# Kernel tuning notes

Hardware: AMD Instinct MI355X
Metric: run time of the kernel (lower is better)

The kernel has to match this reference:

```python
import jax, jax.numpy as jnp
import numpy as np

D_MODEL = 1024
NUM_HEADS = 16
HEAD_DIM = D_MODEL // NUM_HEADS  # 64
B, S = 2, 2048


def setup_inputs() -> dict:
    key = jax.random.key(0)
    k1, k2, k3, k4, k5 = jax.random.split(key, 5)
    scale = 1.0 / np.sqrt(D_MODEL)
    return {
        "x": jax.random.normal(k1, (B, S, D_MODEL), dtype=jnp.float32),
        "Wq": jax.random.normal(k2, (D_MODEL, D_MODEL), dtype=jnp.float32) * scale,
        "bq": jax.random.normal(k3, (D_MODEL,), dtype=jnp.float32) * 0.02,
        "Wv": jax.random.normal(k4, (D_MODEL, D_MODEL), dtype=jnp.float32) * scale,
        "bv": jax.random.normal(k5, (D_MODEL,), dtype=jnp.float32) * 0.02,
    }


def reference(x, Wq, bq, Wv, bv):
    b, s, _ = x.shape
    d, n = HEAD_DIM, NUM_HEADS
    # nn.Linear: y = x @ W.T + b
    Q = x @ Wq.T + bq
    # NOTE (faithful to source bug): K uses the VALUE projection, key weights unused.
    KV = x @ Wv.T + bv
    # einops 'B S (d n) -> B S d n' -> 'B n S d'  (head index n is fast-varying)
    Qh = Q.reshape(b, s, d, n).transpose(0, 3, 1, 2)   # [B, n, S, d]
    Kt = KV.reshape(b, s, d, n).transpose(0, 3, 2, 1)  # [B, n, d, S]
    Vh = KV.reshape(b, s, d, n).transpose(0, 3, 1, 2)  # [B, n, S, d]
    scores = jnp.matmul(Qh, Kt) / jnp.sqrt(jnp.float32(d))  # [B, n, S, S]
    attn = jnp.matmul(jax.nn.softmax(scores, axis=-1), Vh)  # [B, n, S, d]
    # 'B n S d -> B S (n d)'
    out = attn.transpose(0, 2, 1, 3).reshape(b, s, n * d)
    return out
```

## Files before the change

kernel.cpp:

```cpp
#include <hip/hip_runtime.h>
#include <hip/hip_bf16.h>
#include <math.h>


typedef __bf16 bf16x8 __attribute__((ext_vector_type(8)));
typedef float  f32x4  __attribute__((ext_vector_type(4)));
typedef short  s16x4  __attribute__((ext_vector_type(4)));
typedef unsigned short ushort_t;
typedef unsigned short us8 __attribute__((ext_vector_type(8)));

#define QSCALE 0.1803368801111204f

__device__ __forceinline__ unsigned short f2bf(float f) {
  unsigned int u = __builtin_bit_cast(unsigned int, f);
  u += 0x7fffu + ((u >> 16) & 1u);
  return (unsigned short)(u >> 16);
}

__device__ __forceinline__ unsigned int pk2(float a, float b) {
  unsigned int ua = __builtin_bit_cast(unsigned int, a) + 0x8000u;
  unsigned int ub = __builtin_bit_cast(unsigned int, b) + 0x8000u;
  return (ua >> 16) | (ub & 0xffff0000u);
}

__device__ __forceinline__ void gl_lds16(const void* g, void* l) {
  __builtin_amdgcn_global_load_lds(
      (const __attribute__((address_space(1))) unsigned int*)g,
      (__attribute__((address_space(3))) unsigned int*)l, 16, 0, 0);
}

__device__ __forceinline__ f32x4 mfma_k32(bf16x8 a, bf16x8 b, f32x4 c) {
  return __builtin_amdgcn_mfma_f32_16x16x32_bf16(a, b, c, 0, 0, 0);
}
__device__ __forceinline__ f32x4 mfma_k16(s16x4 a, s16x4 b, f32x4 c) {
  return __builtin_amdgcn_mfma_f32_16x16x16bf16_1k(a, b, c, 0, 0, 0);
}

__global__ __launch_bounds__(256) void cvt3_kernel(const float4* __restrict__ x,
                                                   const float4* __restrict__ wq,
                                                   const float4* __restrict__ wv,
                                                   ushort4* __restrict__ dst) {
  const int i = blockIdx.x * 256 + threadIdx.x;
  const float4 v = (i < 1048576) ? x[i]
                 : (i < 1310720) ? wq[i - 1048576]
                                 : wv[i - 1310720];
  ushort4 o;
  o.x = f2bf(v.x); o.y = f2bf(v.y); o.z = f2bf(v.z); o.w = f2bf(v.w);
  dst[i] = o;
}

__global__ __launch_bounds__(256) void proj_kernel(
    const ushort_t* __restrict__ X,
    const ushort_t* __restrict__ Wqm,
    const ushort_t* __restrict__ Wvm,
    const float*    __restrict__ bq,
    const float*    __restrict__ bv,
    ushort_t* __restrict__ Qh,
    ushort_t* __restrict__ KVh,
    ushort_t* __restrict__ KVt)
{
  __shared__ __align__(16) unsigned char lds[32768];
  const int tid = threadIdx.x;
  const int w  = tid >> 6;
  const int l  = tid & 63;
  const int lq = l >> 4;
  const int ll = l & 15;
  const bool isQ = (blockIdx.z == 0);
  const ushort_t* Wmat = isQ ? Wqm : Wvm;
  const float*    bias = isQ ? bq  : bv;
  const int m0 = blockIdx.x * 128;
  const int by = blockIdx.y;
  const int wm = (w & 1) * 64;
  const int wn = (w >> 1) * 64;

  f32x4 acc[4][4] = {};

  for (int k0 = 0; k0 < 1024; k0 += 64) {
    __syncthreads();
#pragma unroll
    for (int t = 0; t < 4; ++t) {
      const int seg = w * 4 + t;
      const int r = seg * 8 + (l >> 3);
      const int cd = (l & 7) ^ (r & 7);
      const int cg = by * 128 + r;
      const int wrow = ((cg & 63) << 4) | (cg >> 6);
      gl_lds16(X    + (size_t)(m0 + r) * 1024 + k0 + cd * 8, lds + seg * 1024);
      gl_lds16(Wmat + (size_t)wrow * 1024 + k0 + cd * 8, lds + 16384 + seg * 1024);
    }
    __syncthreads();
#pragma unroll
    for (int kb = 0; kb < 2; ++kb) {
      const int kc = kb * 4 + lq;
      bf16x8 af[4], bfr[4];
#pragma unroll
      for (int mi = 0; mi < 4; ++mi) {
        const int m = wm + mi * 16 + ll;
        af[mi] = *(const bf16x8*)(lds + m * 128 + ((kc ^ (m & 7)) * 16));
      }
#pragma unroll
      for (int ni = 0; ni < 4; ++ni) {
        const int n = wn + ni * 16 + ll;
        bfr[ni] = *(const bf16x8*)(lds + 16384 + n * 128 + ((kc ^ (n & 7)) * 16));
      }
#pragma unroll
      for (int mi = 0; mi < 4; ++mi)
#pragma unroll
        for (int ni = 0; ni < 4; ++ni)
          acc[mi][ni] = mfma_k32(af[mi], bfr[ni], acc[mi][ni]);
    }
  }

  const int hl = wn >> 6;
  const int hh = by * 2 + hl;
  const int b  = m0 >> 11;
  const int sbase = m0 & 2047;

  if (isQ) {
#pragma unroll
    for (int ni = 0; ni < 4; ++ni) {
      const int ii = ni * 16 + ll;
      const float bb = bias[(ii << 4) | hh];
#pragma unroll
      for (int mi = 0; mi < 4; ++mi)
#pragma unroll
        for (int r = 0; r < 4; ++r) {
          const int s = sbase + wm + mi * 16 + lq * 4 + r;
          const float v = acc[mi][ni][r] + bb;
          Qh[(((size_t)(b * 16 + hh)) * 2048 + s) * 64 + ii] = f2bf(v * QSCALE);
        }
    }
  } else {
    __syncthreads();
#pragma unroll
    for (int ni = 0; ni < 4; ++ni) {
      const int ii = ni * 16 + ll;
      const float bb = bias[(ii << 4) | hh];
#pragma unroll
      for (int mi = 0; mi < 4; ++mi) {
        const float v0 = acc[mi][ni][0] + bb;
        const float v1 = acc[mi][ni][1] + bb;
        const float v2 = acc[mi][ni][2] + bb;
        const float v3 = acc[mi][ni][3] + bb;
        const unsigned int u01 = pk2(v0, v1);
        const unsigned int u23 = pk2(v2, v3);
        const int sl = wm + mi * 16 + lq * 4;
        const size_t kb0 = (((size_t)(b * 16 + hh)) * 2048 + sbase + sl) * 64 + ii;
        KVh[kb0]       = (ushort_t)(u01 & 0xffffu);
        KVh[kb0 + 64]  = (ushort_t)(u01 >> 16);
        KVh[kb0 + 128] = (ushort_t)(u23 & 0xffffu);
        KVh[kb0 + 192] = (ushort_t)(u23 >> 16);
        const int g = (wm >> 2) + mi * 4 + lq;
        const int pc = (g >> 1) ^ ll;
        *(uint2*)(lds + hl * 16384 + ii * 256 + pc * 16 + (g & 1) * 8) =
            make_uint2(u01, u23);
      }
    }
    __syncthreads();
    const int row = tid >> 1;
    const int hl2 = row >> 6, ii2 = row & 63;
    const int cbase = (tid & 1) * 8;
    ushort_t* dst = KVt + (((size_t)(b * 16 + by * 2 + hl2)) * 64 + ii2) * 2048 + sbase;
#pragma unroll
    for (int cc = 0; cc < 8; ++cc) {
      const int c = cbase + cc;
      const int pc = c ^ (ii2 & 15);
      const us8 v = *(const us8*)(lds + hl2 * 16384 + ii2 * 256 + pc * 16);
      *(us8*)(dst + c * 8) = v;
    }
  }
}

__global__ __launch_bounds__(128, 2) void attn_kernel(
    const ushort_t* __restrict__ Qh,
    const ushort_t* __restrict__ KVh,
    const ushort_t* __restrict__ KVt,
    float* __restrict__ out)
{
  __shared__ __align__(16) unsigned char sm[32768];
  const int tid = threadIdx.x;
  const int w  = tid >> 6;
  const int l  = tid & 63;
  const int quad = l >> 4;
  const int ll = l & 15;
  const int bid = blockIdx.x;
  const int bh = ((bid & 7) << 2) | (bid >> 8);
  const int qt = (bid >> 3) & 31;
  const int b = bh >> 4, h = bh & 15;
  const int qw = qt * 64 + w * 32;
  const ushort_t* Qhead  = Qh  + (size_t)bh * (2048 * 64);
  const ushort_t* Khead  = KVh + (size_t)bh * (2048 * 64);
  const ushort_t* Vthead = KVt + (size_t)bh * (64 * 2048);

  bf16x8 qf[2][2];
#pragma unroll
  for (int c = 0; c < 2; ++c)
#pragma unroll
    for (int kb = 0; kb < 2; ++kb)
      qf[c][kb] = *(const bf16x8*)(Qhead + (size_t)(qw + c * 16 + ll) * 64 +
                                   kb * 32 + quad * 8);

  f32x4 O[2][4] = {};
  float l_run[2] = {0.f, 0.f};

  for (int kt = 0; kt < 16; ++kt) {
    const int sk0 = kt * 128;
    __syncthreads();
#pragma unroll
    for (int t = 0; t < 8; ++t) {
      const int seg = w * 8 + t;
      const int r = seg * 8 + (l >> 3);
      const int cd = (l & 7) ^ (r & 7);
      gl_lds16(Khead + (size_t)(sk0 + r) * 64 + cd * 8, sm + seg * 1024);
    }
#pragma unroll
    for (int t = 0; t < 8; ++t) {
      const int seg = w * 8 + t;
      const int d = seg * 4 + (l >> 4);
      const int c8 = (l & 15) ^ (d & 15);
      gl_lds16(Vthead + (size_t)d * 2048 + sk0 + c8 * 8, sm + 16384 + seg * 1024);
    }
    __syncthreads();

    f32x4 Sa[2][8] = {};
#pragma unroll
    for (int kb = 0; kb < 2; ++kb) {
      const int kc = kb * 4 + quad;
#pragma unroll
      for (int ni = 0; ni < 8; ++ni) {
        const int n = ni * 16 + ll;
        const bf16x8 ak = *(const bf16x8*)(sm + n * 128 + ((kc ^ (n & 7)) * 16));
        Sa[0][ni] = mfma_k32(ak, qf[0][kb], Sa[0][ni]);
        Sa[1][ni] = mfma_k32(ak, qf[1][kb], Sa[1][ni]);
      }
    }

    s16x4 pk[2][8];
#pragma unroll
    for (int c = 0; c < 2; ++c) {
      float ps = 0.f;
#pragma unroll
      for (int ni = 0; ni < 8; ++ni) {
        const float p0 = __builtin_amdgcn_exp2f(Sa[c][ni][0]);
        const float p1 = __builtin_amdgcn_exp2f(Sa[c][ni][1]);
        const float p2 = __builtin_amdgcn_exp2f(Sa[c][ni][2]);
        const float p3 = __builtin_amdgcn_exp2f(Sa[c][ni][3]);
        ps += (p0 + p1) + (p2 + p3);
        const uint2 uu = make_uint2(pk2(p0, p1), pk2(p2, p3));
        pk[c][ni] = __builtin_bit_cast(s16x4, uu);
      }
      ps += __shfl_xor(ps, 16);
      ps += __shfl_xor(ps, 32);
      l_run[c] += ps;
    }

#pragma unroll
    for (int ni = 0; ni < 8; ++ni) {
      const int cb = 2 * ni + (quad >> 1);
#pragma unroll
      for (int no = 0; no < 4; ++no) {
        const int row = no * 16 + ll;
        const s16x4 bv = *(const s16x4*)(sm + 16384 + row * 256 +
                                         ((cb ^ ll) * 16) + (quad & 1) * 8);
        O[0][no] = mfma_k16(pk[0][ni], bv, O[0][no]);
        O[1][no] = mfma_k16(pk[1][ni], bv, O[1][no]);
      }
    }
  }

#pragma unroll
  for (int c = 0; c < 2; ++c) {
    const float inv = 1.f / l_run[c];
    float invr[4];
#pragma unroll
    for (int r = 0; r < 4; ++r)
      invr[r] = __shfl(inv, (l & 48) + ((l & 48) >> 2) + r);
    float* op = out + ((size_t)(b * 2048) + qw + c * 16) * 1024 + h * 64;
#pragma unroll
    for (int no = 0; no < 4; ++no)
#pragma unroll
      for (int r = 0; r < 4; ++r) {
        const int q = quad * 4 + r;
        op[(size_t)q * 1024 + no * 16 + ll] = O[c][no][r] * invr[r];
      }
  }
}

extern "C" void kernel_launch(void* const* d_in, const int* in_sizes, int n_in,
                              void* d_out, int out_size, void* d_ws, size_t ws_size,
                              hipStream_t stream) {
  const float* x  = (const float*)d_in[0];
  const float* Wq = (const float*)d_in[1];
  const float* bq = (const float*)d_in[2];
  const float* Wv = (const float*)d_in[3];
  const float* bv = (const float*)d_in[4];
  float* out = (float*)d_out;
  char* ws = (char*)d_ws;

  ushort_t* xbf  = (ushort_t*)(ws);
  ushort_t* wqbf = (ushort_t*)(ws + 8388608);
  ushort_t* wvbf = (ushort_t*)(ws + 10485760);
  ushort_t* Qh   = (ushort_t*)(ws + 12582912);
  ushort_t* KVh  = (ushort_t*)(ws + 20971520);
  ushort_t* KVt  = (ushort_t*)(ws + 29360128);

  cvt3_kernel<<<6144, 256, 0, stream>>>((const float4*)x, (const float4*)Wq,
                                        (const float4*)Wv, (ushort4*)xbf);
  proj_kernel<<<dim3(32, 8, 2), 256, 0, stream>>>(xbf, wqbf, wvbf, bq, bv,
                                                  Qh, KVh, KVt);
  attn_kernel<<<1024, 128, 0, stream>>>(Qh, KVh, KVt, out);
}
```

Measured before the change: 154.8 us.

## Prefetch next K tile during softmax and split barriers with explicit waitcnts

Loads the next K tile into LDS while softmax and PV run on the current tile, and replaces __syncthreads with s_barrier plus targeted vmcnt/lgkmcnt waits so V and K loads overlap compute. It also swaps the manual bf16 packing for the hardware v_cvt_pk_bf16_f32 instruction and moves the row-sum cross-lane shuffles out of the loop to the epilogue. This adds barriers per iteration and relies on hand-counted vmcnt values that must match the issued loads. The hardware conversion rounds to nearest-even, which differs slightly from the previous add-and-truncate rounding.

```diff
diff --git a/kernel.cpp b/kernel.cpp
--- a/kernel.cpp
+++ b/kernel.cpp
@@ -21,6 +21,12 @@
   unsigned int ua = __builtin_bit_cast(unsigned int, a) + 0x8000u;
   unsigned int ub = __builtin_bit_cast(unsigned int, b) + 0x8000u;
   return (ua >> 16) | (ub & 0xffff0000u);
+}
+
+__device__ __forceinline__ unsigned int cvtpk(float lo, float hi) {
+  unsigned int r;
+  asm("v_cvt_pk_bf16_f32 %0, %1, %2" : "=v"(r) : "v"(lo), "v"(hi));
+  return r;
 }
 
 __device__ __forceinline__ void gl_lds16(const void* g, void* l) {
@@ -202,16 +208,20 @@
   f32x4 O[2][4] = {};
   float l_run[2] = {0.f, 0.f};
 
+#pragma unroll
+  for (int t = 0; t < 8; ++t) {
+    const int seg = w * 8 + t;
+    const int r = seg * 8 + (l >> 3);
+    const int cd = (l & 7) ^ (r & 7);
+    gl_lds16(Khead + (size_t)r * 64 + cd * 8, sm + seg * 1024);
+  }
+
   for (int kt = 0; kt < 16; ++kt) {
     const int sk0 = kt * 128;
-    __syncthreads();
-#pragma unroll
-    for (int t = 0; t < 8; ++t) {
-      const int seg = w * 8 + t;
-      const int r = seg * 8 + (l >> 3);
-      const int cd = (l & 7) ^ (r & 7);
-      gl_lds16(Khead + (size_t)(sk0 + r) * 64 + cd * 8, sm + seg * 1024);
-    }
+    asm volatile("s_waitcnt lgkmcnt(0)" ::: "memory");
+    __builtin_amdgcn_sched_barrier(0);
+    __builtin_amdgcn_s_barrier();
+    __builtin_amdgcn_sched_barrier(0);
 #pragma unroll
     for (int t = 0; t < 8; ++t) {
       const int seg = w * 8 + t;
@@ -219,7 +229,10 @@
       const int c8 = (l & 15) ^ (d & 15);
       gl_lds16(Vthead + (size_t)d * 2048 + sk0 + c8 * 8, sm + 16384 + seg * 1024);
     }
-    __syncthreads();
+    asm volatile("s_waitcnt vmcnt(8)" ::: "memory");
+    __builtin_amdgcn_sched_barrier(0);
+    __builtin_amdgcn_s_barrier();
+    __builtin_amdgcn_sched_barrier(0);
 
     f32x4 Sa[2][8] = {};
 #pragma unroll
@@ -231,6 +244,21 @@
         const bf16x8 ak = *(const bf16x8*)(sm + n * 128 + ((kc ^ (n & 7)) * 16));
         Sa[0][ni] = mfma_k32(ak, qf[0][kb], Sa[0][ni]);
         Sa[1][ni] = mfma_k32(ak, qf[1][kb], Sa[1][ni]);
+      }
+    }
+
+    asm volatile("s_waitcnt lgkmcnt(0)" ::: "memory");
+    __builtin_amdgcn_sched_barrier(0);
+    __builtin_amdgcn_s_barrier();
+    __builtin_amdgcn_sched_barrier(0);
+    if (kt < 15) {
+      const int sk1 = sk0 + 128;
+#pragma unroll
+      for (int t = 0; t < 8; ++t) {
+        const int seg = w * 8 + t;
+        const int r = seg * 8 + (l >> 3);
+        const int cd = (l & 7) ^ (r & 7);
+        gl_lds16(Khead + (size_t)(sk1 + r) * 64 + cd * 8, sm + seg * 1024);
       }
     }
 
@@ -245,13 +273,17 @@
         const float p2 = __builtin_amdgcn_exp2f(Sa[c][ni][2]);
         const float p3 = __builtin_amdgcn_exp2f(Sa[c][ni][3]);
         ps += (p0 + p1) + (p2 + p3);
-        const uint2 uu = make_uint2(pk2(p0, p1), pk2(p2, p3));
+        const uint2 uu = make_uint2(cvtpk(p0, p1), cvtpk(p2, p3));
         pk[c][ni] = __builtin_bit_cast(s16x4, uu);
       }
-      ps += __shfl_xor(ps, 16);
-      ps += __shfl_xor(ps, 32);
       l_run[c] += ps;
     }
+
+    if (kt < 15) { asm volatile("s_waitcnt vmcnt(8)" ::: "memory"); }
+    else         { asm volatile("s_waitcnt vmcnt(0)" ::: "memory"); }
+    __builtin_amdgcn_sched_barrier(0);
+    __builtin_amdgcn_s_barrier();
+    __builtin_amdgcn_sched_barrier(0);
 
 #pragma unroll
     for (int ni = 0; ni < 8; ++ni) {
@@ -269,7 +301,10 @@
 
 #pragma unroll
   for (int c = 0; c < 2; ++c) {
-    const float inv = 1.f / l_run[c];
+    float s = l_run[c];
+    s += __shfl_xor(s, 16);
+    s += __shfl_xor(s, 32);
+    const float inv = 1.f / s;
     float invr[4];
 #pragma unroll
     for (int r = 0; r < 4; ++r)
```

After: 154.8 us. No clear change (-0.0%).
